# Kernel tuning notes

Hardware: AMD Instinct MI355X
Metric: run time of the kernel (lower is better)

The kernel has to match this reference:

```python
import jax, jax.numpy as jnp
import numpy as np
import math

B, T, E = 2, 2048, 1024
H = 16
D = E // H  # head_dim = 64

def setup_inputs() -> dict:
    key = jax.random.key(0)
    k1, k2, k3, k4, k5 = jax.random.split(key, 5)
    s = 0.02
    return {
        "x": jax.random.normal(k1, (B, T, E), dtype=jnp.float32),
        "W_attn": jax.random.normal(k2, (E, 3 * E), dtype=jnp.float32) * s,
        "b_attn": jax.random.normal(k3, (3 * E,), dtype=jnp.float32) * s,
        "W_proj": jax.random.normal(k4, (E, E), dtype=jnp.float32) * s,
        "b_proj": jax.random.normal(k5, (E,), dtype=jnp.float32) * s,
    }

def reference(x, W_attn, b_attn, W_proj, b_proj):
    Bx, Tx, Ex = x.shape
    qkv = x @ W_attn + b_attn                      # [B,T,3E]
    q, k, v = jnp.split(qkv, 3, axis=2)
    # [B,T,E] -> [B,H,T,D]
    def heads(t):
        return t.reshape(Bx, Tx, H, D).transpose(0, 2, 1, 3)
    q, k, v = heads(q), heads(k), heads(v)
    scores = jnp.einsum('bhqd,bhkd->bhqk', q, k) / math.sqrt(D)
    causal = jnp.tril(jnp.ones((Tx, Tx), dtype=bool))
    scores = jnp.where(causal, scores, -jnp.inf)
    attn = jax.nn.softmax(scores, axis=-1)
    out = jnp.einsum('bhqk,bhkd->bhqd', attn, v)   # [B,H,T,D]
    out = out.transpose(0, 2, 1, 3).reshape(Bx, Tx, Ex)
    return out @ W_proj + b_proj
```

## Files before the change

kernel.cpp:

```cpp
#include <hip/hip_runtime.h>


typedef unsigned short u16;
typedef unsigned int u32;
typedef __bf16 bf8 __attribute__((ext_vector_type(8)));
typedef float f32x4 __attribute__((ext_vector_type(4)));
typedef float f32x16 __attribute__((ext_vector_type(16)));
typedef u32 u32x4v __attribute__((ext_vector_type(4)));

__device__ __forceinline__ u16 f2b(float f) {
    return __builtin_bit_cast(u16, (__bf16)f);
}

__device__ __forceinline__ u32 pk2(float lo, float hi) {
    return (u32)f2b(lo) | ((u32)f2b(hi) << 16);
}

__device__ __forceinline__ f32x4 mfma16(bf8 a, bf8 b, f32x4 c) {
    return __builtin_amdgcn_mfma_f32_16x16x32_bf16(a, b, c, 0, 0, 0);
}

__device__ __forceinline__ f32x16 mfma32(bf8 a, bf8 b, f32x16 c) {
    return __builtin_amdgcn_mfma_f32_32x32x16_bf16(a, b, c, 0, 0, 0);
}

__device__ __forceinline__ float fexp2(float x) {
    return __builtin_amdgcn_exp2f(x);
}

__device__ __forceinline__ void pl32swap(u32& a, u32& b) {
    asm("v_permlane32_swap_b32 %0, %1" : "+v"(a), "+v"(b));
}

__device__ __forceinline__ void gload_lds16(const u16* g, u16* l) {
    __builtin_amdgcn_global_load_lds(
        (__attribute__((address_space(1))) void*)(g),
        (__attribute__((address_space(3))) void*)(l), 16, 0, 0);
}

__global__ __launch_bounds__(256) void k_prep(const float* __restrict__ x,
                                              const float* __restrict__ Wa,
                                              const float* __restrict__ Wp,
                                              u16* __restrict__ Xb,
                                              u16* __restrict__ WtA,
                                              u16* __restrict__ WtP) {
    __shared__ float tile[64][65];
    int id = blockIdx.x, t = threadIdx.x;
    if (id < 4096) {
        int i = id * 256 + t;
        float4 v = ((const float4*)x)[i];
        ushort4 o;
        o.x = f2b(v.x); o.y = f2b(v.y); o.z = f2b(v.z); o.w = f2b(v.w);
        ((ushort4*)Xb)[i] = o;
        return;
    }
    const float* in; u16* out; int N, j;
    if (id < 4864) { j = id - 4096; in = Wa; out = WtA; N = 3072; }
    else           { j = id - 4864; in = Wp; out = WtP; N = 1024; }
    int k0 = (j & 15) * 64, n0 = (j >> 4) * 64;
    int c = t & 63, r0 = t >> 6;
#pragma unroll
    for (int i = 0; i < 16; ++i) {
        int r = r0 + i * 4;
        tile[r][c] = in[(size_t)(k0 + r) * N + n0 + c];
    }
    __syncthreads();
#pragma unroll
    for (int i = 0; i < 16; ++i) {
        int r = r0 + i * 4;
        out[(size_t)(n0 + r) * 1024 + k0 + c] = f2b(tile[c][r]);
    }
}

#define GEMM_STAGE(GA0, GA1, GB0, GB1, K, B)                                   \
    do {                                                                       \
        gload_lds16(GA0 + (K), As[B] + tid * 8);                               \
        gload_lds16(GA1 + (K), As[B] + (256 + tid) * 8);                       \
        gload_lds16(GB0 + (K), Bs[B] + tid * 8);                               \
        gload_lds16(GB1 + (K), Bs[B] + (256 + tid) * 8);                       \
    } while (0)

#define GEMM_CORE(Aptr, Bptr)                                                  \
    int tid = threadIdx.x;                                                     \
    int w = tid >> 6, lane = tid & 63, l16 = lane & 15, quad = lane >> 4;      \
    int m0 = blockIdx.x * 128, n0 = blockIdx.y * 128;                          \
    int wr = (w >> 1) * 64, wc = (w & 1) * 64;                                 \
    __shared__ u16 As[2][128 * 32];                                            \
    __shared__ u16 Bs[2][128 * 32];                                            \
    f32x4 acc[4][4];                                                           \
    _Pragma("unroll") for (int mi = 0; mi < 4; ++mi)                           \
        _Pragma("unroll") for (int ni = 0; ni < 4; ++ni)                       \
            _Pragma("unroll") for (int r = 0; r < 4; ++r) acc[mi][ni][r] = 0.f;\
    int srow0 = tid >> 2, srow1 = 64 + srow0;                                  \
    int slc = ((tid & 3) ^ ((tid >> 3) & 3)) * 8;      \
    const u16* gA0 = Aptr + (size_t)(m0 + srow0) * 1024 + slc;                 \
    const u16* gA1 = Aptr + (size_t)(m0 + srow1) * 1024 + slc;                 \
    const u16* gB0 = Bptr + (size_t)(n0 + srow0) * 1024 + slc;                 \
    const u16* gB1 = Bptr + (size_t)(n0 + srow1) * 1024 + slc;                 \
    int cq = (quad ^ ((l16 >> 1) & 3)) * 8;               \
    GEMM_STAGE(gA0, gA1, gB0, gB1, 0, 0);                                      \
    for (int it = 0; it < 32; ++it) {                                          \
        int pb = it & 1;                                                       \
        __syncthreads();                           \
        bf8 af[4], bf[4];                                                      \
        _Pragma("unroll") for (int mi = 0; mi < 4; ++mi)                       \
            af[mi] = *(const bf8*)(As[pb] + (wr + mi * 16 + l16) * 32 + cq);   \
        _Pragma("unroll") for (int ni = 0; ni < 4; ++ni)                       \
            bf[ni] = *(const bf8*)(Bs[pb] + (wc + ni * 16 + l16) * 32 + cq);   \
        if (it < 31) GEMM_STAGE(gA0, gA1, gB0, gB1, (it + 1) * 32, pb ^ 1);    \
        _Pragma("unroll") for (int mi = 0; mi < 4; ++mi)                       \
            _Pragma("unroll") for (int ni = 0; ni < 4; ++ni)                   \
                acc[mi][ni] = mfma16(af[mi], bf[ni], acc[mi][ni]);             \
    }

__global__ __launch_bounds__(256, 3) void k_qkv(const u16* __restrict__ Xb,
                                                const u16* __restrict__ WtA,
                                                const float* __restrict__ ba,
                                                u16* __restrict__ Qb,
                                                u16* __restrict__ Kb,
                                                u16* __restrict__ Vtb) {
    GEMM_CORE(Xb, WtA)
    int sel = n0 >> 10;
    u16* dst = sel == 0 ? Qb : (sel == 1 ? Kb : Vtb);
    const float qs = 0.18033688011112042f;
#pragma unroll
    for (int ni = 0; ni < 4; ++ni) {
        int n = n0 + wc + ni * 16 + l16;
        float bias = ba[n];
        int h = (n & 1023) >> 6;
        int d = n & 63;
#pragma unroll
        for (int mi = 0; mi < 4; ++mi)
#pragma unroll
            for (int r = 0; r < 4; ++r) {
                int m = m0 + wr + mi * 16 + quad * 4 + r;
                int bb = m >> 11, tt = m & 2047;
                float v = acc[mi][ni][r] + bias;
                size_t hb = (size_t)(bb * 16 + h);
                if (sel == 2)
                    dst[hb * 131072 + (size_t)(tt >> 6) * 4096 + d * 64 + (tt & 63)] = f2b(v);
                else
                    dst[(hb * 2048 + tt) * 64 + d] =
                        f2b(sel == 0 ? v * qs : v);
            }
    }
}

__global__ __launch_bounds__(256, 3) void k_proj(const u16* __restrict__ AO,
                                                 const u16* __restrict__ WtP,
                                                 const float* __restrict__ bp,
                                                 float* __restrict__ out) {
    GEMM_CORE(AO, WtP)
#pragma unroll
    for (int ni = 0; ni < 4; ++ni) {
        int n = n0 + wc + ni * 16 + l16;
        float bias = bp[n];
#pragma unroll
        for (int mi = 0; mi < 4; ++mi)
#pragma unroll
            for (int r = 0; r < 4; ++r) {
                int m = m0 + wr + mi * 16 + quad * 4 + r;
                out[(size_t)m * 1024 + n] = acc[mi][ni][r] + bias;
            }
    }
}


#define STAGE128(KT2, B) do {                                                 \
    const u16* kt_ = Kh + (size_t)(KT2) * 8192;                               \
    _Pragma("unroll") for (int i_ = 0; i_ < 4; ++i_) {                        \
        int ci_ = i_ * 256 + tid;             \
        gload_lds16(kt_ + (ci_ >> 3) * 64 +                                   \
                    (((ci_ & 7) ^ ((ci_ >> 3) & 7)) * 8), Ks[B] + ci_ * 8);   \
    }                                                                         \
    const u16* vt_ = Vh + (size_t)(KT2) * 8192;                               \
    _Pragma("unroll") for (int i_ = 0; i_ < 4; ++i_) {                        \
        int ci_ = i_ * 256 + tid;                  \
        gload_lds16(vt_ + (ci_ >> 3) * 64 +                                   \
                    (((ci_ & 7) ^ ((ci_ >> 3) & 7)) * 8), Vs[B] + ci_ * 8);   \
    }                                                                         \
} while (0)

#define PVSTEP(SG, BFR) do {                                                  \
    bf8 va_ = *(const bf8*)(vb_ + l31 * 64 + (((2 * (SG) + h) ^ swz) * 8));   \
    bf8 vc_ = *(const bf8*)(vb_ + (32 + l31) * 64 +                           \
                            (((2 * (SG) + h) ^ swz) * 8));                    \
    bf8 pf_ = __builtin_bit_cast(bf8, BFR);                                   \
    oT0 = mfma32(va_, pf_, oT0);                                              \
    oT1 = mfma32(vc_, pf_, oT1);                                              \
} while (0)

#define REPACK_PV(ST, SG0, SG1) do {                                          \
    u32 pk_[8];                                                               \
    _Pragma("unroll") for (int j = 0; j < 8; ++j)                             \
        pk_[j] = pk2(ST[2 * j], ST[2 * j + 1]);                               \
    pl32swap(pk_[0], pk_[2]); pl32swap(pk_[1], pk_[3]);                       \
    pl32swap(pk_[4], pk_[6]); pl32swap(pk_[5], pk_[7]);                       \
    u32x4v f0_ = {pk_[0], pk_[1], pk_[2], pk_[3]};                            \
    u32x4v f1_ = {pk_[4], pk_[5], pk_[6], pk_[7]};                            \
    PVSTEP(SG0, f0_);                                                         \
    PVSTEP(SG1, f1_);                                                         \
} while (0)

#define TREE16(S)                                                             \
    (((((S)[0] + (S)[1]) + ((S)[2] + (S)[3])) +                               \
      (((S)[4] + (S)[5]) + ((S)[6] + (S)[7]))) +                              \
     ((((S)[8] + (S)[9]) + ((S)[10] + (S)[11])) +                             \
      (((S)[12] + (S)[13]) + ((S)[14] + (S)[15]))))

__global__ __launch_bounds__(256, 2) void k_attn(const u16* __restrict__ Qb,
                                                 const u16* __restrict__ Kb,
                                                 const u16* __restrict__ Vtb,
                                                 u16* __restrict__ AO) {
    int id = blockIdx.x;
    int bh = (id & 7) * 4 + ((id >> 3) & 3);
    int t  = 15 - (id >> 5);
    int tid = threadIdx.x;
    int w = tid >> 6, lane = tid & 63, l31 = lane & 31, h = lane >> 5;

    const u16* Qh = Qb  + (size_t)bh * 131072;
    const u16* Kh = Kb  + (size_t)bh * 131072;
    const u16* Vh = Vtb + (size_t)bh * 131072;

    __shared__ u16 Ks[2][8192];
    __shared__ u16 Vs[2][8192];

    int tq = 4 * t + w;
    int qr = tq * 32;
    int ktmax = tq >> 1;
    int nk2 = t + 1;

    bf8 qf[4];
#pragma unroll
    for (int s = 0; s < 4; ++s)
        qf[s] = *(const bf8*)(Qh + (size_t)(qr + l31) * 64 + s * 16 + h * 8);

    float l_acc = 0.f;
    f32x16 oT0, oT1;
#pragma unroll
    for (int r = 0; r < 16; ++r) { oT0[r] = 0.f; oT1[r] = 0.f; }

    int swz = l31 & 7;

    STAGE128(0, 0);
    for (int k2 = 0; k2 < nk2; ++k2) {
        int pb = k2 & 1;
        __syncthreads();
        if (k2 + 1 < nk2) STAGE128(k2 + 1, pb ^ 1);

#pragma unroll
        for (int s = 0; s < 2; ++s) {
            int kt = 2 * k2 + s;
            if (kt > ktmax) continue;
            const u16* kb_ = Ks[pb] + s * 4096;
            const u16* vb_ = Vs[pb] + s * 4096;
            bool diag = (kt == ktmax);
            bool doK1 = !(diag && ((tq & 1) == 0));

            f32x16 sT0, sT1;
#pragma unroll
            for (int r = 0; r < 16; ++r) { sT0[r] = 0.f; sT1[r] = 0.f; }
#pragma unroll
            for (int d = 0; d < 4; ++d) {
                bf8 kf = *(const bf8*)(kb_ + l31 * 64 +
                                       (((2 * d + h) ^ swz) * 8));
                sT0 = mfma32(kf, qf[d], sT0);
            }
            if (doK1) {
#pragma unroll
                for (int d = 0; d < 4; ++d) {
                    bf8 kf = *(const bf8*)(kb_ + (32 + l31) * 64 +
                                           (((2 * d + h) ^ swz) * 8));
                    sT1 = mfma32(kf, qf[d], sT1);
                }
            }

            int kb0 = kt * 64, qg = qr + l31;
            if (diag) {
#pragma unroll
                for (int r = 0; r < 16; ++r) {
                    int krow = kb0 + (r & 3) + 8 * (r >> 2) + 4 * h;
                    sT0[r] = fexp2(krow <= qg ? sT0[r] : -1e30f);
                }
                if (doK1) {
#pragma unroll
                    for (int r = 0; r < 16; ++r) {
                        int krow = kb0 + 32 + (r & 3) + 8 * (r >> 2) + 4 * h;
                        sT1[r] = fexp2(krow <= qg ? sT1[r] : -1e30f);
                    }
                }
            } else {
#pragma unroll
                for (int r = 0; r < 16; ++r) sT0[r] = fexp2(sT0[r]);
#pragma unroll
                for (int r = 0; r < 16; ++r) sT1[r] = fexp2(sT1[r]);
            }
            l_acc += TREE16(sT0);
            if (doK1) l_acc += TREE16(sT1);

            REPACK_PV(sT0, 0, 1);
            if (doK1) REPACK_PV(sT1, 2, 3);
        }
    }

    __syncthreads();
    float lsum = l_acc + __shfl_xor(l_acc, 32, 64);
    float linv = __builtin_amdgcn_rcpf(lsum);

    u32* Ot = (u32*)(&Ks[0][0]) + w * 1152;
#pragma unroll
    for (int j = 0; j < 8; ++j) {
        int col = 4 * (j >> 1) + 2 * h + (j & 1);
        Ot[l31 * 36 + col]      = pk2(oT0[2 * j] * linv, oT0[2 * j + 1] * linv);
        Ot[l31 * 36 + 16 + col] = pk2(oT1[2 * j] * linv, oT1[2 * j + 1] * linv);
    }
    asm volatile("s_waitcnt lgkmcnt(0)" ::: "memory");
    __builtin_amdgcn_sched_barrier(0);

    int q2 = lane >> 1, half = lane & 1;
    int eb = bh >> 4, eh = bh & 15;
    size_t row = (size_t)eb * 2048 + qr + q2;
    const u32* src = Ot + q2 * 36 + half * 16;
    u32* dstg = (u32*)(AO + row * 1024 + eh * 64) + half * 16;
#pragma unroll
    for (int c = 0; c < 4; ++c)
        *(u32x4v*)(dstg + 4 * c) = *(const u32x4v*)(src + 4 * c);
}

extern "C" void kernel_launch(void* const* d_in, const int* in_sizes, int n_in,
                              void* d_out, int out_size, void* d_ws, size_t ws_size,
                              hipStream_t stream) {
    const float* x  = (const float*)d_in[0];
    const float* Wa = (const float*)d_in[1];
    const float* ba = (const float*)d_in[2];
    const float* Wp = (const float*)d_in[3];
    const float* bp = (const float*)d_in[4];
    float* out = (float*)d_out;

    char* ws = (char*)d_ws;
    const size_t MB = 1024 * 1024;
    u16* Xb  = (u16*)(ws);
    u16* WtA = (u16*)(ws + 8  * MB);
    u16* WtP = (u16*)(ws + 14 * MB);
    u16* Qb  = (u16*)(ws + 16 * MB);
    u16* Kb  = (u16*)(ws + 24 * MB);
    u16* Vtb = (u16*)(ws + 32 * MB);
    u16* AO  = Xb;

    k_prep<<<dim3(5120),    dim3(256), 0, stream>>>(x, Wa, Wp, Xb, WtA, WtP);
    k_qkv <<<dim3(32, 24),  dim3(256), 0, stream>>>(Xb, WtA, ba, Qb, Kb, Vtb);
    k_attn<<<dim3(512),     dim3(256), 0, stream>>>(Qb, Kb, Vtb, AO);
    k_proj<<<dim3(32, 8),   dim3(256), 0, stream>>>(AO, WtP, bp, out);
}
```

Measured before the change: 174.1 us.

## Split key tiles across two wave groups in attention and reduce via LDS

Doubles the attention block to 512 threads. Each 128-key stage is split so one wave group processes the first 64 keys and the other the second 64, instead of one group doing both sequentially. At the end, the second group writes its partial output and row sum to shared memory and the first group adds them before normalizing. This aims to raise parallelism and latency hiding per block, at the cost of an extra LDS reduction, more barriers, and higher register and occupancy pressure under the new launch bounds.

```diff
diff --git a/kernel.cpp b/kernel.cpp
--- a/kernel.cpp
+++ b/kernel.cpp
@@ -168,16 +168,15 @@
 
 #define STAGE128(KT2, B) do {                                                 \
     const u16* kt_ = Kh + (size_t)(KT2) * 8192;                               \
-    _Pragma("unroll") for (int i_ = 0; i_ < 4; ++i_) {                        \
-        int ci_ = i_ * 256 + tid;             \
+    const u16* vt_ = Vh + (size_t)(KT2) * 8192;                               \
+    _Pragma("unroll") for (int i_ = 0; i_ < 2; ++i_) {                        \
+        int ci_ = i_ * 512 + tid;             \
         gload_lds16(kt_ + (ci_ >> 3) * 64 +                                   \
-                    (((ci_ & 7) ^ ((ci_ >> 3) & 7)) * 8), Ks[B] + ci_ * 8);   \
-    }                                                                         \
-    const u16* vt_ = Vh + (size_t)(KT2) * 8192;                               \
-    _Pragma("unroll") for (int i_ = 0; i_ < 4; ++i_) {                        \
-        int ci_ = i_ * 256 + tid;                  \
+                    (((ci_ & 7) ^ ((ci_ >> 3) & 7)) * 8),                     \
+                    SMEM[B][0] + ci_ * 8);                                    \
         gload_lds16(vt_ + (ci_ >> 3) * 64 +                                   \
-                    (((ci_ & 7) ^ ((ci_ >> 3) & 7)) * 8), Vs[B] + ci_ * 8);   \
+                    (((ci_ & 7) ^ ((ci_ >> 3) & 7)) * 8),                     \
+                    SMEM[B][1] + ci_ * 8);                                    \
     }                                                                         \
 } while (0)
 
@@ -208,7 +207,7 @@
      ((((S)[8] + (S)[9]) + ((S)[10] + (S)[11])) +                             \
       (((S)[12] + (S)[13]) + ((S)[14] + (S)[15]))))
 
-__global__ __launch_bounds__(256, 2) void k_attn(const u16* __restrict__ Qb,
+__global__ __launch_bounds__(512, 4) void k_attn(const u16* __restrict__ Qb,
                                                  const u16* __restrict__ Kb,
                                                  const u16* __restrict__ Vtb,
                                                  u16* __restrict__ AO) {
@@ -217,15 +216,15 @@
     int t  = 15 - (id >> 5);
     int tid = threadIdx.x;
     int w = tid >> 6, lane = tid & 63, l31 = lane & 31, h = lane >> 5;
+    int wq = w & 3, p = w >> 2;
 
     const u16* Qh = Qb  + (size_t)bh * 131072;
     const u16* Kh = Kb  + (size_t)bh * 131072;
     const u16* Vh = Vtb + (size_t)bh * 131072;
 
-    __shared__ u16 Ks[2][8192];
-    __shared__ u16 Vs[2][8192];
-
-    int tq = 4 * t + w;
+    __shared__ u16 SMEM[2][2][8192];
+
+    int tq = 4 * t + wq;
     int qr = tq * 32;
     int ktmax = tq >> 1;
     int nk2 = t + 1;
@@ -248,12 +247,10 @@
         __syncthreads();
         if (k2 + 1 < nk2) STAGE128(k2 + 1, pb ^ 1);
 
-#pragma unroll
-        for (int s = 0; s < 2; ++s) {
-            int kt = 2 * k2 + s;
-            if (kt > ktmax) continue;
-            const u16* kb_ = Ks[pb] + s * 4096;
-            const u16* vb_ = Vs[pb] + s * 4096;
+        int kt = 2 * k2 + p;
+        if (kt <= ktmax) {
+            const u16* kb_ = SMEM[pb][0] + p * 4096;
+            const u16* vb_ = SMEM[pb][1] + p * 4096;
             bool diag = (kt == ktmax);
             bool doK1 = !(diag && ((tq & 1) == 0));
 
@@ -304,10 +301,25 @@
     }
 
     __syncthreads();
+    float* comb = (float*)&SMEM[0][0][0];
+    if (p == 1) {
+        float* cw = comb + (wq * 64 + lane) * 36;
+#pragma unroll
+        for (int r = 0; r < 16; ++r) { cw[r] = oT0[r]; cw[16 + r] = oT1[r]; }
+        cw[32] = l_acc;
+    }
+    __syncthreads();
+    if (p == 1) return;
+
+    const float* cr = comb + (wq * 64 + lane) * 36;
+#pragma unroll
+    for (int r = 0; r < 16; ++r) { oT0[r] += cr[r]; oT1[r] += cr[16 + r]; }
+    l_acc += cr[32];
+
     float lsum = l_acc + __shfl_xor(l_acc, 32, 64);
     float linv = __builtin_amdgcn_rcpf(lsum);
 
-    u32* Ot = (u32*)(&Ks[0][0]) + w * 1152;
+    u32* Ot = (u32*)&SMEM[0][0][0] + 9216 + wq * 1152;
 #pragma unroll
     for (int j = 0; j < 8; ++j) {
         int col = 4 * (j >> 1) + 2 * h + (j & 1);
@@ -349,6 +361,6 @@
 
     k_prep<<<dim3(5120),    dim3(256), 0, stream>>>(x, Wa, Wp, Xb, WtA, WtP);
     k_qkv <<<dim3(32, 24),  dim3(256), 0, stream>>>(Xb, WtA, ba, Qb, Kb, Vtb);
-    k_attn<<<dim3(512),     dim3(256), 0, stream>>>(Qb, Kb, Vtb, AO);
+    k_attn<<<dim3(512),     dim3(512), 0, stream>>>(Qb, Kb, Vtb, AO);
     k_proj<<<dim3(32, 8),   dim3(256), 0, stream>>>(AO, WtP, bp, out);
 }
```

Result: no change. 173.3 us (median of 2 runs) (-0.5%).

## Split attention blocks to 64 query rows with 64-key staging tiles

Applied to the files above, without the earlier changes.

The attention kernel moves from 256-thread blocks covering 128 query rows to 128-thread blocks covering 64 query rows, and doubles the grid to 1024 blocks. K/V staging drops from 128-key double buffers to 64-key tiles, which halves shared memory per block. The goal is finer-grained, better-balanced work across CUs for the causal triangle and more resident blocks. In exchange, each staged K/V tile is reused by half as many waves, so L2/global traffic rises and there are more barriers per unit of work.

```diff
diff --git a/kernel.cpp b/kernel.cpp
--- a/kernel.cpp
+++ b/kernel.cpp
@@ -166,18 +166,17 @@
 }
 
 
-#define STAGE128(KT2, B) do {                                                 \
-    const u16* kt_ = Kh + (size_t)(KT2) * 8192;                               \
+#define STAGE64(KT, B) do {                                                   \
+    const u16* kt_ = Kh + (size_t)(KT) * 4096;                                \
+    const u16* vt_ = Vh + (size_t)(KT) * 4096;                                \
     _Pragma("unroll") for (int i_ = 0; i_ < 4; ++i_) {                        \
-        int ci_ = i_ * 256 + tid;             \
+        int ci_ = i_ * 128 + tid;             \
         gload_lds16(kt_ + (ci_ >> 3) * 64 +                                   \
-                    (((ci_ & 7) ^ ((ci_ >> 3) & 7)) * 8), Ks[B] + ci_ * 8);   \
-    }                                                                         \
-    const u16* vt_ = Vh + (size_t)(KT2) * 8192;                               \
-    _Pragma("unroll") for (int i_ = 0; i_ < 4; ++i_) {                        \
-        int ci_ = i_ * 256 + tid;                  \
+                    (((ci_ & 7) ^ ((ci_ >> 3) & 7)) * 8),                     \
+                    SMEM[B][0] + ci_ * 8);                                    \
         gload_lds16(vt_ + (ci_ >> 3) * 64 +                                   \
-                    (((ci_ & 7) ^ ((ci_ >> 3) & 7)) * 8), Vs[B] + ci_ * 8);   \
+                    (((ci_ & 7) ^ ((ci_ >> 3) & 7)) * 8),                     \
+                    SMEM[B][1] + ci_ * 8);                                    \
     }                                                                         \
 } while (0)
 
@@ -208,13 +207,13 @@
      ((((S)[8] + (S)[9]) + ((S)[10] + (S)[11])) +                             \
       (((S)[12] + (S)[13]) + ((S)[14] + (S)[15]))))
 
-__global__ __launch_bounds__(256, 2) void k_attn(const u16* __restrict__ Qb,
+__global__ __launch_bounds__(128, 2) void k_attn(const u16* __restrict__ Qb,
                                                  const u16* __restrict__ Kb,
                                                  const u16* __restrict__ Vtb,
                                                  u16* __restrict__ AO) {
     int id = blockIdx.x;
     int bh = (id & 7) * 4 + ((id >> 3) & 3);
-    int t  = 15 - (id >> 5);
+    int tp = 31 - (id >> 5);
     int tid = threadIdx.x;
     int w = tid >> 6, lane = tid & 63, l31 = lane & 31, h = lane >> 5;
 
@@ -222,13 +221,12 @@
     const u16* Kh = Kb  + (size_t)bh * 131072;
     const u16* Vh = Vtb + (size_t)bh * 131072;
 
-    __shared__ u16 Ks[2][8192];
-    __shared__ u16 Vs[2][8192];
-
-    int tq = 4 * t + w;
+    __shared__ u16 SMEM[2][2][4096];
+
+    int tq = 2 * tp + w;
     int qr = tq * 32;
-    int ktmax = tq >> 1;
-    int nk2 = t + 1;
+    int ktmax = tp;
+    int nkt = tp + 1;
 
     bf8 qf[4];
 #pragma unroll
@@ -242,72 +240,68 @@
 
     int swz = l31 & 7;
 
-    STAGE128(0, 0);
-    for (int k2 = 0; k2 < nk2; ++k2) {
-        int pb = k2 & 1;
+    STAGE64(0, 0);
+    for (int s = 0; s < nkt; ++s) {
+        int pb = s & 1;
         __syncthreads();
-        if (k2 + 1 < nk2) STAGE128(k2 + 1, pb ^ 1);
-
-#pragma unroll
-        for (int s = 0; s < 2; ++s) {
-            int kt = 2 * k2 + s;
-            if (kt > ktmax) continue;
-            const u16* kb_ = Ks[pb] + s * 4096;
-            const u16* vb_ = Vs[pb] + s * 4096;
-            bool diag = (kt == ktmax);
-            bool doK1 = !(diag && ((tq & 1) == 0));
-
-            f32x16 sT0, sT1;
-#pragma unroll
-            for (int r = 0; r < 16; ++r) { sT0[r] = 0.f; sT1[r] = 0.f; }
+        if (s + 1 < nkt) STAGE64(s + 1, pb ^ 1);
+
+        const u16* kb_ = SMEM[pb][0];
+        const u16* vb_ = SMEM[pb][1];
+        bool diag = (s == ktmax);
+        bool doK1 = !(diag && ((tq & 1) == 0));
+        int kb0 = s * 64;
+
+        f32x16 sT0, sT1;
+#pragma unroll
+        for (int r = 0; r < 16; ++r) { sT0[r] = 0.f; sT1[r] = 0.f; }
+#pragma unroll
+        for (int d = 0; d < 4; ++d) {
+            bf8 kf = *(const bf8*)(kb_ + l31 * 64 + (((2 * d + h) ^ swz) * 8));
+            sT0 = mfma32(kf, qf[d], sT0);
+        }
+        if (doK1) {
 #pragma unroll
             for (int d = 0; d < 4; ++d) {
-                bf8 kf = *(const bf8*)(kb_ + l31 * 64 +
+                bf8 kf = *(const bf8*)(kb_ + (32 + l31) * 64 +
                                        (((2 * d + h) ^ swz) * 8));
-                sT0 = mfma32(kf, qf[d], sT0);
+                sT1 = mfma32(kf, qf[d], sT1);
+            }
+        }
+
+        int qg = qr + l31;
+        if (diag) {
+#pragma unroll
+            for (int r = 0; r < 16; ++r) {
+                int krow = kb0 + (r & 3) + 8 * (r >> 2) + 4 * h;
+                sT0[r] = fexp2(krow <= qg ? sT0[r] : -1e30f);
             }
             if (doK1) {
 #pragma unroll
-                for (int d = 0; d < 4; ++d) {
-                    bf8 kf = *(const bf8*)(kb_ + (32 + l31) * 64 +
-                                           (((2 * d + h) ^ swz) * 8));
-                    sT1 = mfma32(kf, qf[d], sT1);
+                for (int r = 0; r < 16; ++r) {
+                    int krow = kb0 + 32 + (r & 3) + 8 * (r >> 2) + 4 * h;
+                    sT1[r] = fexp2(krow <= qg ? sT1[r] : -1e30f);
                 }
             }
-
-            int kb0 = kt * 64, qg = qr + l31;
-            if (diag) {
-#pragma unroll
-                for (int r = 0; r < 16; ++r) {
-                    int krow = kb0 + (r & 3) + 8 * (r >> 2) + 4 * h;
-                    sT0[r] = fexp2(krow <= qg ? sT0[r] : -1e30f);
-                }
-                if (doK1) {
-#pragma unroll
-                    for (int r = 0; r < 16; ++r) {
-                        int krow = kb0 + 32 + (r & 3) + 8 * (r >> 2) + 4 * h;
-                        sT1[r] = fexp2(krow <= qg ? sT1[r] : -1e30f);
-                    }
-                }
-            } else {
-#pragma unroll
-                for (int r = 0; r < 16; ++r) sT0[r] = fexp2(sT0[r]);
-#pragma unroll
-                for (int r = 0; r < 16; ++r) sT1[r] = fexp2(sT1[r]);
-            }
-            l_acc += TREE16(sT0);
-            if (doK1) l_acc += TREE16(sT1);
-
-            REPACK_PV(sT0, 0, 1);
-            if (doK1) REPACK_PV(sT1, 2, 3);
+        } else {
+#pragma unroll
+            for (int r = 0; r < 16; ++r) sT0[r] = fexp2(sT0[r]);
+#pragma unroll
+            for (int r = 0; r < 16; ++r) sT1[r] = fexp2(sT1[r]);
         }
+        l_acc += TREE16(sT0);
+        if (doK1) l_acc += TREE16(sT1);
+
+        REPACK_PV(sT0, 0, 1);
+        if (doK1) REPACK_PV(sT1, 2, 3);
     }
 
     __syncthreads();
+
     float lsum = l_acc + __shfl_xor(l_acc, 32, 64);
     float linv = __builtin_amdgcn_rcpf(lsum);
 
-    u32* Ot = (u32*)(&Ks[0][0]) + w * 1152;
+    u32* Ot = (u32*)&SMEM[0][0][0] + w * 1152;
 #pragma unroll
     for (int j = 0; j < 8; ++j) {
         int col = 4 * (j >> 1) + 2 * h + (j & 1);
@@ -349,6 +343,6 @@
 
     k_prep<<<dim3(5120),    dim3(256), 0, stream>>>(x, Wa, Wp, Xb, WtA, WtP);
     k_qkv <<<dim3(32, 24),  dim3(256), 0, stream>>>(Xb, WtA, ba, Qb, Kb, Vtb);
-    k_attn<<<dim3(512),     dim3(256), 0, stream>>>(Qb, Kb, Vtb, AO);
+    k_attn<<<dim3(1024),    dim3(128), 0, stream>>>(Qb, Kb, Vtb, AO);
     k_proj<<<dim3(32, 8),   dim3(256), 0, stream>>>(AO, WtP, bp, out);
 }
```

Measured after the change: 179.5 us. +3.1%, slower.
